# Kernel tuning notes

Hardware: AMD Instinct MI355X
Metric: run time of the kernel (lower is better)

## Reference

```python
import jax, jax.numpy as jnp
import numpy as np

B, IN, H, NB = 8192, 1024, 2048, 8
BS = H // NB  # 256


def setup_inputs() -> dict:
    key = jax.random.key(0)
    ks = jax.random.split(key, 4)
    s = 0.02
    return {
        "x": jax.random.normal(ks[0], (B, IN), dtype=jnp.float32),
        "h": jax.random.normal(ks[1], (B, H), dtype=jnp.float32),
        "W_ir": jax.random.normal(ks[2], (3 * H, IN), dtype=jnp.float32) * s,
        "b_ir_lin": jnp.zeros((3 * H,), dtype=jnp.float32),
        "b_ir": jnp.zeros((3 * H,), dtype=jnp.float32),
        "W_h": jax.random.normal(ks[3], (NB, 3 * BS, BS), dtype=jnp.float32) * s,
        "b_hr": jnp.zeros((3 * H,), dtype=jnp.float32),
    }


def reference(x, h, W_ir, b_ir_lin, b_ir, W_h, b_hr):
    b = x.shape[0]
    nb, three_bs, bs = W_h.shape
    hdim = nb * bs
    # input projection: w_ir(x) + b_ir  -> [B, 3H], chunked globally into r,z,n
    wx = x @ W_ir.T + b_ir_lin + b_ir
    wxr, wxz, wxn = jnp.split(wx, 3, axis=1)
    wxr = wxr.reshape(b, nb, bs)
    wxz = wxz.reshape(b, nb, bs)
    wxn = wxn.reshape(b, nb, bs)
    # block-diagonal hidden projection: per-block Linear(bs -> 3*bs), no bias
    hb = h.reshape(b, nb, bs)
    # b_hr is sliced in contiguous chunks of 3*bs per block (local r,z,n layout)
    wh = jnp.einsum('bki,koi->bko', hb, W_h) + b_hr.reshape(nb, three_bs)
    whr, whz, whn = jnp.split(wh, 3, axis=2)
    r = jax.nn.sigmoid(wxr + whr)
    z = jax.nn.sigmoid(wxz + whz)
    n = jnp.tanh(wxn + r * whn)
    h_new = (1.0 - z) * hb + z * n
    return h_new.reshape(b, hdim)
```

## Files before the change

kernel.cpp:

```cpp
#include <hip/hip_runtime.h>
#include <cstdint>
#include <cstddef>


typedef __attribute__((ext_vector_type(8))) short bf16x8;
typedef __attribute__((ext_vector_type(4))) float f32x4;

__device__ __forceinline__ unsigned short f2bf(float f) {
    uint32_t u = __float_as_uint(f);
    u += 0x7FFFu + ((u >> 16) & 1u);
    return (unsigned short)(u >> 16);
}
__device__ __forceinline__ float bf2f(unsigned short b) {
    return __uint_as_float(((uint32_t)b) << 16);
}

__device__ __forceinline__ void gload16(const void* g, void* l) {
    __builtin_amdgcn_global_load_lds(
        (const __attribute__((address_space(1))) void*)g,
        (__attribute__((address_space(3))) void*)l,
        16, 0, 0);
}

__device__ __forceinline__ float sigmoidf_(float x) {
    return 1.0f / (1.0f + __expf(-x));
}
__device__ __forceinline__ float tanhf_(float x) {
    float e = __expf(-2.0f * fabsf(x));
    float t = (1.0f - e) / (1.0f + e);
    return copysignf(t, x);
}

__global__ __launch_bounds__(256)
void cast_all(const float* __restrict__ x, const float* __restrict__ wir,
              const float* __restrict__ h, const float* __restrict__ wh,
              unsigned short* __restrict__ xb, unsigned short* __restrict__ wirb,
              unsigned short* __restrict__ hb, unsigned short* __restrict__ whb) {
    const int i = blockIdx.x * 256 + threadIdx.x;
    const float* s; unsigned short* d; int j;
    if (i < 2097152)      { s = x;   d = xb;   j = i; }
    else if (i < 3670016) { s = wir; d = wirb; j = i - 2097152; }
    else if (i < 7864320) { s = h;   d = hb;   j = i - 3670016; }
    else                  { s = wh;  d = whb;  j = i - 7864320; }
    const float4 v = *reinterpret_cast<const float4*>(s + (size_t)j * 4);
    ushort4 o;
    o.x = f2bf(v.x); o.y = f2bf(v.y); o.z = f2bf(v.z); o.w = f2bf(v.w);
    *reinterpret_cast<ushort4*>(d + (size_t)j * 4) = o;
}


#define MM24(AV, BV, NT) do {                                                  \
    _Pragma("unroll")                                                          \
    for (int m_ = 0; m_ < 4; ++m_) {                                           \
        acc[0][m_][0] = __builtin_amdgcn_mfma_f32_16x16x32_bf16(               \
            AV[m_], BV[0][0], acc[0][m_][0], 0, 0, 0);                         \
        acc[0][m_][1] = __builtin_amdgcn_mfma_f32_16x16x32_bf16(               \
            AV[m_], BV[0][1], acc[0][m_][1], 0, 0, 0);                         \
        acc[1][m_][0] = __builtin_amdgcn_mfma_f32_16x16x32_bf16(               \
            AV[m_], BV[1][0], acc[1][m_][0], 0, 0, 0);                         \
        acc[1][m_][1] = __builtin_amdgcn_mfma_f32_16x16x32_bf16(               \
            AV[m_], BV[1][1], acc[1][m_][1], 0, 0, 0);                         \
        acc[NT][m_][0] = __builtin_amdgcn_mfma_f32_16x16x32_bf16(              \
            AV[m_], BV[2][0], acc[NT][m_][0], 0, 0, 0);                        \
        acc[NT][m_][1] = __builtin_amdgcn_mfma_f32_16x16x32_bf16(              \
            AV[m_], BV[2][1], acc[NT][m_][1], 0, 0, 0);                        \
    }                                                                          \
} while (0)

#define RDSET(AV, BV, sl, kbx) do {                                            \
    _Pragma("unroll")                                                          \
    for (int m_ = 0; m_ < 4; ++m_)                                             \
        AV[m_] = *(const bf16x8*)(pAr[sl] + m_ * 1024 + (kbx));                \
    _Pragma("unroll")                                                          \
    for (int s_ = 0; s_ < 3; ++s_) {                                           \
        BV[s_][0] = *(const bf16x8*)(pBr[sl] + s_ * 4096 + (kbx));             \
        BV[s_][1] = *(const bf16x8*)(pBr[sl] + s_ * 4096 + 1024 + (kbx));      \
    }                                                                          \
} while (0)

#define SGB_HALF() do {                                                        \
    __builtin_amdgcn_sched_group_barrier(0x010, 5, 0);                         \
    _Pragma("unroll")                                                          \
    for (int g_ = 0; g_ < 5; ++g_) {                                           \
        __builtin_amdgcn_sched_group_barrier(0x100, 2, 0);                     \
        __builtin_amdgcn_sched_group_barrier(0x008, 5, 0);                     \
    }                                                                          \
} while (0)

#define I_1(kt, ds) do {                                                       \
    gload16(XbB  + 0 * 32768   + (kt) * 64, As + (ds) * 8192 + 0 * 2048 + doff); \
    gload16(XbB  + 1 * 32768   + (kt) * 64, As + (ds) * 8192 + 1 * 2048 + doff); \
    gload16(XbB  + 2 * 32768   + (kt) * 64, As + (ds) * 8192 + 2 * 2048 + doff); \
    gload16(XbB  + 3 * 32768   + (kt) * 64, As + (ds) * 8192 + 3 * 2048 + doff); \
    gload16(WirB + 0 * 2097152 + 0 * 32768 + (kt) * 64, Bs + (ds) * 12288 + 0 * 2048 + doff); \
    gload16(WirB + 0 * 2097152 + 1 * 32768 + (kt) * 64, Bs + (ds) * 12288 + 1 * 2048 + doff); \
    gload16(WirB + 1 * 2097152 + 0 * 32768 + (kt) * 64, Bs + (ds) * 12288 + 2 * 2048 + doff); \
    gload16(WirB + 1 * 2097152 + 1 * 32768 + (kt) * 64, Bs + (ds) * 12288 + 3 * 2048 + doff); \
    gload16(WirB + 2 * 2097152 + 0 * 32768 + (kt) * 64, Bs + (ds) * 12288 + 4 * 2048 + doff); \
    gload16(WirB + 2 * 2097152 + 1 * 32768 + (kt) * 64, Bs + (ds) * 12288 + 5 * 2048 + doff); \
} while (0)
#define I_2(k2, ds) do {                                                       \
    gload16(XhB + 0 * 65536 + (k2) * 64, As + (ds) * 8192 + 0 * 2048 + doff);  \
    gload16(XhB + 1 * 65536 + (k2) * 64, As + (ds) * 8192 + 1 * 2048 + doff);  \
    gload16(XhB + 2 * 65536 + (k2) * 64, As + (ds) * 8192 + 2 * 2048 + doff);  \
    gload16(XhB + 3 * 65536 + (k2) * 64, As + (ds) * 8192 + 3 * 2048 + doff);  \
    gload16(WhB + 0 * 65536 + 0 * 8192 + (k2) * 64, Bs + (ds) * 12288 + 0 * 2048 + doff); \
    gload16(WhB + 0 * 65536 + 1 * 8192 + (k2) * 64, Bs + (ds) * 12288 + 1 * 2048 + doff); \
    gload16(WhB + 1 * 65536 + 0 * 8192 + (k2) * 64, Bs + (ds) * 12288 + 2 * 2048 + doff); \
    gload16(WhB + 1 * 65536 + 1 * 8192 + (k2) * 64, Bs + (ds) * 12288 + 3 * 2048 + doff); \
    gload16(WhB + 2 * 65536 + 0 * 8192 + (k2) * 64, Bs + (ds) * 12288 + 4 * 2048 + doff); \
    gload16(WhB + 2 * 65536 + 1 * 8192 + (k2) * 64, Bs + (ds) * 12288 + 5 * 2048 + doff); \
} while (0)

#define BODY(sl, STAGE, NTp, NTc) do {                                         \
    asm volatile("s_waitcnt lgkmcnt(0)" ::: "memory");                         \
    asm volatile("s_waitcnt vmcnt(0)" ::: "memory");                           \
    __builtin_amdgcn_s_barrier();                                              \
    STAGE;                                                                     \
    RDSET(avA, bvA, sl, kb0);                                                  \
    MM24(avB, bvB, NTp);                                                       \
    SGB_HALF();                                                                \
    RDSET(avB, bvB, sl, kb1);                                                  \
    MM24(avA, bvA, NTc);                                                       \
    SGB_HALF();                                                                \
    __builtin_amdgcn_sched_barrier(0);                                         \
} while (0)

__global__ __launch_bounds__(256, 2)
void gru_fused(const unsigned short* __restrict__ Xb,
               const unsigned short* __restrict__ Wirb,
               const unsigned short* __restrict__ Hbb,
               const unsigned short* __restrict__ Whb,
               const float* __restrict__ b_ir_lin,
               const float* __restrict__ b_ir,
               const float* __restrict__ b_hr,
               float* __restrict__ out) {
    constexpr int K1 = 1024, H = 2048;
    __shared__ unsigned short lds[2 * 8192 + 2 * 12288];
    unsigned short* const As = lds;
    unsigned short* const Bs = lds + 2 * 8192;

    const int tid  = threadIdx.x;
    const int lane = tid & 63;
    const int w    = tid >> 6;
    const int wm   = w >> 1;
    const int wn   = w & 1;

    const int bid  = blockIdx.x;
    const int kb   = bid & 7;
    const int idx  = bid >> 3;
    const int bm   = (idx >> 2) * 128;
    const int hsub = idx & 3;
    const int hcb  = kb * 256 + hsub * 64;

    const int srow  = tid >> 3;
    const int chunk = (tid & 7) ^ (srow & 7);
    const int scol  = chunk * 8;
    const int doff  = tid * 8;
    const unsigned short* XbB  = Xb   + (size_t)(bm + srow) * K1 + scol;
    const unsigned short* WirB = Wirb + (size_t)(hcb + srow) * K1 + scol;
    const unsigned short* XhB  = Hbb  + (size_t)(bm + srow) * H + kb * 256 + scol;
    const unsigned short* WhB  = Whb  + (size_t)kb * 196608
                                      + (size_t)(hsub * 64 + srow) * 256 + scol;

    const int fr  = lane & 15;
    const int k0e = (lane >> 4) * 8;
    const int mfr = (fr & 7) << 4;
    const int kb0 = ((k0e * 2) ^ mfr) >> 1;
    const int kb1 = (((k0e * 2) + 64) ^ mfr) >> 1;
    const unsigned short* pAr[2];
    const unsigned short* pBr[2];
    pAr[0] = As + (wm * 64 + fr) * 64;
    pAr[1] = As + 8192 + (wm * 64 + fr) * 64;
    pBr[0] = Bs + (wn * 32 + fr) * 64;
    pBr[1] = Bs + 12288 + (wn * 32 + fr) * 64;

    f32x4 acc[4][4][2] = {};
    bf16x8 avA[4], avB[4], bvA[3][2], bvB[3][2];

    I_1(0, 0);
    asm volatile("s_waitcnt vmcnt(0)" ::: "memory");
    __builtin_amdgcn_s_barrier();
    I_1(1, 1);
    RDSET(avA, bvA, 0, kb0);
    RDSET(avB, bvB, 0, kb1);
    MM24(avA, bvA, 2);

    BODY(1, I_1(2, 0),  2, 2);
    BODY(0, I_1(3, 1),  2, 2);
    BODY(1, I_1(4, 0),  2, 2);
    BODY(0, I_1(5, 1),  2, 2);
    BODY(1, I_1(6, 0),  2, 2);
    BODY(0, I_1(7, 1),  2, 2);
    BODY(1, I_1(8, 0),  2, 2);
    BODY(0, I_1(9, 1),  2, 2);
    BODY(1, I_1(10, 0), 2, 2);
    BODY(0, I_1(11, 1), 2, 2);
    BODY(1, I_1(12, 0), 2, 2);
    BODY(0, I_1(13, 1), 2, 2);
    BODY(1, I_1(14, 0), 2, 2);
    BODY(0, I_1(15, 1), 2, 2);
    BODY(1, I_2(0, 0),  2, 2);
    BODY(0, I_2(1, 1),  2, 3);
    BODY(1, I_2(2, 0),  3, 3);
    BODY(0, I_2(3, 1),  3, 3);
    BODY(1, ((void)0),  3, 3);
    asm volatile("s_waitcnt lgkmcnt(0)" ::: "memory");
    MM24(avB, bvB, 3);

    const int rq = (lane >> 4) * 4;
    #pragma unroll
    for (int n = 0; n < 2; ++n) {
        const int hcol = hcb + wn * 32 + n * 16 + fr;
        const int lcol = hcol & 255;
        const float bir0 = b_ir_lin[hcol]        + b_ir[hcol];
        const float bir1 = b_ir_lin[2048 + hcol] + b_ir[2048 + hcol];
        const float bir2 = b_ir_lin[4096 + hcol] + b_ir[4096 + hcol];
        const float bhr0 = b_hr[kb * 768 + lcol];
        const float bhr1 = b_hr[kb * 768 + 256 + lcol];
        const float bhr2 = b_hr[kb * 768 + 512 + lcol];
        #pragma unroll
        for (int mi = 0; mi < 4; ++mi) {
            #pragma unroll
            for (int r = 0; r < 4; ++r) {
                const int row = bm + wm * 64 + mi * 16 + rq + r;
                const float pr = acc[0][mi][n][r] + bir0 + bhr0;
                const float pz = acc[1][mi][n][r] + bir1 + bhr1;
                const float xn = acc[2][mi][n][r] + bir2;
                const float hn = acc[3][mi][n][r] + bhr2;
                const float rg = sigmoidf_(pr);
                const float zg = sigmoidf_(pz);
                const float ng = tanhf_(xn + rg * hn);
                const float hv = bf2f(Hbb[(size_t)row * H + hcol]);
                out[(size_t)row * H + hcol] = (1.0f - zg) * hv + zg * ng;
            }
        }
    }
}

extern "C" void kernel_launch(void* const* d_in, const int* in_sizes, int n_in,
                              void* d_out, int out_size, void* d_ws, size_t ws_size,
                              hipStream_t stream) {
    const float* x        = (const float*)d_in[0];
    const float* h        = (const float*)d_in[1];
    const float* W_ir     = (const float*)d_in[2];
    const float* b_ir_lin = (const float*)d_in[3];
    const float* b_ir     = (const float*)d_in[4];
    const float* W_h      = (const float*)d_in[5];
    const float* b_hr     = (const float*)d_in[6];
    float* out = (float*)d_out;

    char* ws = (char*)d_ws;
    unsigned short* xb   = (unsigned short*)(ws);
    unsigned short* wirb = (unsigned short*)(ws + 16777216);
    unsigned short* hb   = (unsigned short*)(ws + 29360128);
    unsigned short* whb  = (unsigned short*)(ws + 62914560);

    cast_all<<<32256, 256, 0, stream>>>(x, W_ir, h, W_h, xb, wirb, hb, whb);

    gru_fused<<<2048, 256, 0, stream>>>(xb, wirb, hb, whb,
                                        b_ir_lin, b_ir, b_hr, out);
}
```

Baseline: 167.0 us.

## Fuse h fp32-to-bf16 conversion into GEMM loader, drop h from cast kernel

```diff
diff --git a/kernel.cpp b/kernel.cpp
--- a/kernel.cpp
+++ b/kernel.cpp
@@ -10,9 +10,6 @@
     uint32_t u = __float_as_uint(f);
     u += 0x7FFFu + ((u >> 16) & 1u);
     return (unsigned short)(u >> 16);
-}
-__device__ __forceinline__ float bf2f(unsigned short b) {
-    return __uint_as_float(((uint32_t)b) << 16);
 }
 
 __device__ __forceinline__ void gload16(const void* g, void* l) {
@@ -33,15 +30,14 @@
 
 __global__ __launch_bounds__(256)
 void cast_all(const float* __restrict__ x, const float* __restrict__ wir,
-              const float* __restrict__ h, const float* __restrict__ wh,
+              const float* __restrict__ wh,
               unsigned short* __restrict__ xb, unsigned short* __restrict__ wirb,
-              unsigned short* __restrict__ hb, unsigned short* __restrict__ whb) {
+              unsigned short* __restrict__ whb) {
     const int i = blockIdx.x * 256 + threadIdx.x;
     const float* s; unsigned short* d; int j;
     if (i < 2097152)      { s = x;   d = xb;   j = i; }
     else if (i < 3670016) { s = wir; d = wirb; j = i - 2097152; }
-    else if (i < 7864320) { s = h;   d = hb;   j = i - 3670016; }
-    else                  { s = wh;  d = whb;  j = i - 7864320; }
+    else                  { s = wh;  d = whb;  j = i - 3670016; }
     const float4 v = *reinterpret_cast<const float4*>(s + (size_t)j * 4);
     ushort4 o;
     o.x = f2bf(v.x); o.y = f2bf(v.y); o.z = f2bf(v.z); o.w = f2bf(v.w);
@@ -79,7 +75,7 @@
 } while (0)
 
 #define SGB_HALF() do {                                                        \
-    __builtin_amdgcn_sched_group_barrier(0x010, 5, 0);                         \
+    __builtin_amdgcn_sched_group_barrier(0x030, 5, 0);                         \
     _Pragma("unroll")                                                          \
     for (int g_ = 0; g_ < 5; ++g_) {                                           \
         __builtin_amdgcn_sched_group_barrier(0x100, 2, 0);                     \
@@ -99,11 +95,7 @@
     gload16(WirB + 2 * 2097152 + 0 * 32768 + (kt) * 64, Bs + (ds) * 12288 + 4 * 2048 + doff); \
     gload16(WirB + 2 * 2097152 + 1 * 32768 + (kt) * 64, Bs + (ds) * 12288 + 5 * 2048 + doff); \
 } while (0)
-#define I_2(k2, ds) do {                                                       \
-    gload16(XhB + 0 * 65536 + (k2) * 64, As + (ds) * 8192 + 0 * 2048 + doff);  \
-    gload16(XhB + 1 * 65536 + (k2) * 64, As + (ds) * 8192 + 1 * 2048 + doff);  \
-    gload16(XhB + 2 * 65536 + (k2) * 64, As + (ds) * 8192 + 2 * 2048 + doff);  \
-    gload16(XhB + 3 * 65536 + (k2) * 64, As + (ds) * 8192 + 3 * 2048 + doff);  \
+#define IB2(k2, ds) do {                                                       \
     gload16(WhB + 0 * 65536 + 0 * 8192 + (k2) * 64, Bs + (ds) * 12288 + 0 * 2048 + doff); \
     gload16(WhB + 0 * 65536 + 1 * 8192 + (k2) * 64, Bs + (ds) * 12288 + 1 * 2048 + doff); \
     gload16(WhB + 1 * 65536 + 0 * 8192 + (k2) * 64, Bs + (ds) * 12288 + 2 * 2048 + doff); \
@@ -111,8 +103,25 @@
     gload16(WhB + 2 * 65536 + 0 * 8192 + (k2) * 64, Bs + (ds) * 12288 + 4 * 2048 + doff); \
     gload16(WhB + 2 * 65536 + 1 * 8192 + (k2) * 64, Bs + (ds) * 12288 + 5 * 2048 + doff); \
 } while (0)
-
-#define BODY(sl, STAGE, NTp, NTc) do {                                         \
+#define LOADH(k2) do {                                                         \
+    _Pragma("unroll") for (int q_ = 0; q_ < 4; ++q_) {                         \
+        hf[q_][0] = *(const float4*)(HfB + (size_t)q_ * 32 * H + (k2) * 64);   \
+        hf[q_][1] = *(const float4*)(HfB + (size_t)q_ * 32 * H + (k2) * 64 + 4); \
+    }                                                                          \
+} while (0)
+#define WRITEH(ds) do {                                                        \
+    _Pragma("unroll") for (int q_ = 0; q_ < 4; ++q_) {                         \
+        bf16x8 o_;                                                             \
+        o_[0] = (short)f2bf(hf[q_][0].x); o_[1] = (short)f2bf(hf[q_][0].y);    \
+        o_[2] = (short)f2bf(hf[q_][0].z); o_[3] = (short)f2bf(hf[q_][0].w);    \
+        o_[4] = (short)f2bf(hf[q_][1].x); o_[5] = (short)f2bf(hf[q_][1].y);    \
+        o_[6] = (short)f2bf(hf[q_][1].z); o_[7] = (short)f2bf(hf[q_][1].w);    \
+        *(bf16x8*)(As + (ds) * 8192 + q_ * 2048 + wof) = o_;                   \
+    }                                                                          \
+} while (0)
+#define IH2(k2, ds) do { LOADH(k2); IB2(k2, ds); } while (0)
+
+#define BODY(sl, STAGE, WMID, NTp, NTc) do {                                   \
     asm volatile("s_waitcnt lgkmcnt(0)" ::: "memory");                         \
     asm volatile("s_waitcnt vmcnt(0)" ::: "memory");                           \
     __builtin_amdgcn_s_barrier();                                              \
@@ -120,6 +129,7 @@
     RDSET(avA, bvA, sl, kb0);                                                  \
     MM24(avB, bvB, NTp);                                                       \
     SGB_HALF();                                                                \
+    WMID;                                                                      \
     RDSET(avB, bvB, sl, kb1);                                                  \
     MM24(avA, bvA, NTc);                                                       \
     SGB_HALF();                                                                \
@@ -129,7 +139,7 @@
 __global__ __launch_bounds__(256, 2)
 void gru_fused(const unsigned short* __restrict__ Xb,
                const unsigned short* __restrict__ Wirb,
-               const unsigned short* __restrict__ Hbb,
+               const float* __restrict__ Hf,
                const unsigned short* __restrict__ Whb,
                const float* __restrict__ b_ir_lin,
                const float* __restrict__ b_ir,
@@ -159,9 +169,10 @@
     const int doff  = tid * 8;
     const unsigned short* XbB  = Xb   + (size_t)(bm + srow) * K1 + scol;
     const unsigned short* WirB = Wirb + (size_t)(hcb + srow) * K1 + scol;
-    const unsigned short* XhB  = Hbb  + (size_t)(bm + srow) * H + kb * 256 + scol;
     const unsigned short* WhB  = Whb  + (size_t)kb * 196608
                                       + (size_t)(hsub * 64 + srow) * 256 + scol;
+    const float* HfB = Hf + (size_t)(bm + srow) * H + kb * 256 + (tid & 7) * 8;
+    const int wof = (srow * 8 + ((tid & 7) ^ (srow & 7))) * 8;
 
     const int fr  = lane & 15;
     const int k0e = (lane >> 4) * 8;
@@ -177,6 +188,7 @@
 
     f32x4 acc[4][4][2] = {};
     bf16x8 avA[4], avB[4], bvA[3][2], bvB[3][2];
+    float4 hf[4][2];
 
     I_1(0, 0);
     asm volatile("s_waitcnt vmcnt(0)" ::: "memory");
@@ -186,25 +198,25 @@
     RDSET(avB, bvB, 0, kb1);
     MM24(avA, bvA, 2);
 
-    BODY(1, I_1(2, 0),  2, 2);
-    BODY(0, I_1(3, 1),  2, 2);
-    BODY(1, I_1(4, 0),  2, 2);
-    BODY(0, I_1(5, 1),  2, 2);
-    BODY(1, I_1(6, 0),  2, 2);
-    BODY(0, I_1(7, 1),  2, 2);
-    BODY(1, I_1(8, 0),  2, 2);
-    BODY(0, I_1(9, 1),  2, 2);
-    BODY(1, I_1(10, 0), 2, 2);
-    BODY(0, I_1(11, 1), 2, 2);
-    BODY(1, I_1(12, 0), 2, 2);
-    BODY(0, I_1(13, 1), 2, 2);
-    BODY(1, I_1(14, 0), 2, 2);
-    BODY(0, I_1(15, 1), 2, 2);
-    BODY(1, I_2(0, 0),  2, 2);
-    BODY(0, I_2(1, 1),  2, 3);
-    BODY(1, I_2(2, 0),  3, 3);
-    BODY(0, I_2(3, 1),  3, 3);
-    BODY(1, ((void)0),  3, 3);
+    BODY(1, I_1(2, 0),  ((void)0), 2, 2);
+    BODY(0, I_1(3, 1),  ((void)0), 2, 2);
+    BODY(1, I_1(4, 0),  ((void)0), 2, 2);
+    BODY(0, I_1(5, 1),  ((void)0), 2, 2);
+    BODY(1, I_1(6, 0),  ((void)0), 2, 2);
+    BODY(0, I_1(7, 1),  ((void)0), 2, 2);
+    BODY(1, I_1(8, 0),  ((void)0), 2, 2);
+    BODY(0, I_1(9, 1),  ((void)0), 2, 2);
+    BODY(1, I_1(10, 0), ((void)0), 2, 2);
+    BODY(0, I_1(11, 1), ((void)0), 2, 2);
+    BODY(1, I_1(12, 0), ((void)0), 2, 2);
+    BODY(0, I_1(13, 1), ((void)0), 2, 2);
+    BODY(1, I_1(14, 0), ((void)0), 2, 2);
+    BODY(0, I_1(15, 1), ((void)0), 2, 2);
+    BODY(1, IH2(0, 0),  WRITEH(0), 2, 2);
+    BODY(0, IH2(1, 1),  WRITEH(1), 2, 3);
+    BODY(1, IH2(2, 0),  WRITEH(0), 3, 3);
+    BODY(0, IH2(3, 1),  WRITEH(1), 3, 3);
+    BODY(1, ((void)0),  ((void)0), 3, 3);
     asm volatile("s_waitcnt lgkmcnt(0)" ::: "memory");
     MM24(avB, bvB, 3);
 
@@ -231,7 +243,7 @@
                 const float rg = sigmoidf_(pr);
                 const float zg = sigmoidf_(pz);
                 const float ng = tanhf_(xn + rg * hn);
-                const float hv = bf2f(Hbb[(size_t)row * H + hcol]);
+                const float hv = Hf[(size_t)row * H + hcol];
                 out[(size_t)row * H + hcol] = (1.0f - zg) * hv + zg * ng;
             }
         }
@@ -253,11 +265,10 @@
     char* ws = (char*)d_ws;
     unsigned short* xb   = (unsigned short*)(ws);
     unsigned short* wirb = (unsigned short*)(ws + 16777216);
-    unsigned short* hb   = (unsigned short*)(ws + 29360128);
-    unsigned short* whb  = (unsigned short*)(ws + 62914560);
-
-    cast_all<<<32256, 256, 0, stream>>>(x, W_ir, h, W_h, xb, wirb, hb, whb);
-
-    gru_fused<<<2048, 256, 0, stream>>>(xb, wirb, hb, whb,
+    unsigned short* whb  = (unsigned short*)(ws + 29360128);
+
+    cast_all<<<15872, 256, 0, stream>>>(x, W_ir, W_h, xb, wirb, whb);
+
+    gru_fused<<<2048, 256, 0, stream>>>(xb, wirb, h, whb,
                                         b_ir_lin, b_ir, b_hr, out);
 }
```

Measured after the change: 159.6 us. 1.05x faster.
